# Performance work log

Hardware: AMD Instinct MI355X
Metric: run time of the kernel (lower is better)

Reference implementation:

```python
import jax, jax.numpy as jnp
import numpy as np

B, LQ, LK, D = 8, 2048, 2048, 1024


def setup_inputs() -> dict:
    key = jax.random.key(0)
    k1, k2, k3, k4, k5 = jax.random.split(key, 5)
    inp = jax.random.normal(k1, (B, LQ, D), dtype=jnp.float32)
    memory = jax.random.normal(k2, (B, LK, D), dtype=jnp.float32)
    # 0/1 float mask over memory positions (1 = masked out)
    mask = (jax.random.uniform(k3, (B, LK)) < 0.15).astype(jnp.float32)
    # nn.Linear(D, 1, bias=False): weight shape [1, D], kaiming-uniform-ish init
    w_input = jax.random.uniform(k4, (1, D), dtype=jnp.float32,
                                 minval=-1.0 / np.sqrt(D), maxval=1.0 / np.sqrt(D))
    # dot_scale ~ U(0, 1/sqrt(D)) per original .uniform_(1/input_size**0.5)
    dot_scale = jax.random.uniform(k5, (D,), dtype=jnp.float32,
                                   minval=0.0, maxval=1.0 / np.sqrt(D))
    return {"input": inp, "memory": memory, "mask": mask,
            "w_input": w_input, "dot_scale": dot_scale}


def reference(input, memory, mask, w_input, dot_scale):
    # input_dot: Linear(D,1,bias=False) -> [B, Lq, 1]
    input_dot = jnp.einsum('bqd,od->bqo', input, w_input)  # o == 1
    # cross_dot: (input * dot_scale) @ memory^T -> [B, Lq, Lk]
    cross_dot = jnp.einsum('bqd,bkd->bqk', input * dot_scale, memory)
    att = input_dot + cross_dot - 1e30 * mask[:, None, :]
    weight_one = jax.nn.softmax(att, axis=-1)  # [B, Lq, Lk]
    output_one = jnp.einsum('bqk,bkd->bqd', weight_one, memory)
    return output_one
```

## Files before the change

kernel.cpp:

```cpp
#include <hip/hip_runtime.h>

#define B_  8
#define LQ_ 2048
#define LK_ 2048
#define D_  1024

typedef unsigned short u16;
using short8  = __attribute__((ext_vector_type(8))) short;
using floatx4 = __attribute__((ext_vector_type(4))) float;

#define GAS __attribute__((address_space(1)))
#define LAS __attribute__((address_space(3)))

__device__ __forceinline__ u16 f2bf(float f) {
  unsigned u = __float_as_uint(f);
  u += 0x7fffu + ((u >> 16) & 1u);
  return (u16)(u >> 16);
}
__device__ __forceinline__ float bf2f(u16 h) {
  return __uint_as_float(((unsigned)h) << 16);
}

__global__ void prep(const float* __restrict__ in, const float* __restrict__ mem,
                     const float* __restrict__ ds, u16* __restrict__ qb,
                     u16* __restrict__ mb, u16* __restrict__ mbT) {
  __shared__ u16 tile[64][68];
  int tid = threadIdx.x;
  int tx = tid & 15, ty = tid >> 4;
  int b = blockIdx.z;

  if (blockIdx.y < 16) {
    int k0 = blockIdx.x * 64, d0 = blockIdx.y * 64;
    const float* mB = mem + (size_t)b * LK_ * D_;
    u16* mbB = mb  + (size_t)b * LK_ * D_;
    u16* mtB = mbT + (size_t)b * D_ * LK_;
#pragma unroll
    for (int i = 0; i < 4; i++) {
      int r = ty + 16 * i;
      float4 v = *(const float4*)(mB + (size_t)(k0 + r) * D_ + d0 + tx * 4);
      ushort4 h;
      h.x = f2bf(v.x); h.y = f2bf(v.y); h.z = f2bf(v.z); h.w = f2bf(v.w);
      *(ushort4*)(mbB + (size_t)(k0 + r) * D_ + d0 + tx * 4) = h;
      *(ushort4*)(&tile[r][tx * 4]) = h;
    }
    __syncthreads();
#pragma unroll
    for (int i = 0; i < 4; i++) {
      int rr = ty + 16 * i;
      ushort4 o;
      o.x = tile[tx * 4 + 0][rr];
      o.y = tile[tx * 4 + 1][rr];
      o.z = tile[tx * 4 + 2][rr];
      o.w = tile[tx * 4 + 3][rr];
      *(ushort4*)(mtB + (size_t)(d0 + rr) * LK_ + k0 + tx * 4) = o;
    }
  } else {
    int q0 = blockIdx.x * 64, d0 = (blockIdx.y - 16) * 64;
    const float* iB = in + (size_t)b * LQ_ * D_;
    u16* qB = qb + (size_t)b * LQ_ * D_;
    float4 s4 = *(const float4*)(ds + d0 + tx * 4);
#pragma unroll
    for (int i = 0; i < 4; i++) {
      int r = ty + 16 * i;
      float4 v = *(const float4*)(iB + (size_t)(q0 + r) * D_ + d0 + tx * 4);
      ushort4 h;
      h.x = f2bf(v.x * s4.x); h.y = f2bf(v.y * s4.y);
      h.z = f2bf(v.z * s4.z); h.w = f2bf(v.w * s4.w);
      *(ushort4*)(qB + (size_t)(q0 + r) * D_ + d0 + tx * 4) = h;
    }
  }
}

template <int MODE>
__global__ void gemm_bt(const u16* __restrict__ A, const u16* __restrict__ Bm,
                        void* __restrict__ C, const float* __restrict__ mask,
                        int K, int lda, int ldb, int ldc,
                        size_t sA, size_t sB, size_t sC) {
  __shared__ __align__(16) u16 As[128 * 32];
  __shared__ __align__(16) u16 Bs[128 * 32];
  int tid = threadIdx.x;
  int lane = tid & 63, w = tid >> 6;
  int wm = (w >> 1) * 64, wn = (w & 1) * 64;
  int lm = lane & 15, quad = lane >> 4;

  int tiles_n = gridDim.x;
  int bid = (blockIdx.z * gridDim.y + blockIdx.y) * tiles_n + blockIdx.x;
  int bz = bid & 7;
  int s = bid >> 3;
  const int GM = 8;
  int per_group = GM * tiles_n;
  int group = s / per_group;
  int rem = s - group * per_group;
  int tm = group * GM + (rem & (GM - 1));
  int tn = rem >> 3;

  const u16* Ab = A  + (size_t)bz * sA + (size_t)(tm * 128) * lda;
  const u16* Bb = Bm + (size_t)bz * sB + (size_t)(tn * 128) * ldb;

  int c0 = tid, c1 = tid + 256;
  const u16* gA0 = Ab + (size_t)(c0 >> 2) * lda + (c0 & 3) * 8;
  const u16* gA1 = Ab + (size_t)(c1 >> 2) * lda + (c1 & 3) * 8;
  const u16* gB0 = Bb + (size_t)(c0 >> 2) * ldb + (c0 & 3) * 8;
  const u16* gB1 = Bb + (size_t)(c1 >> 2) * ldb + (c1 & 3) * 8;
  u16* lA0 = As + c0 * 8; u16* lA1 = As + c1 * 8;
  u16* lB0 = Bs + c0 * 8; u16* lB1 = Bs + c1 * 8;

  floatx4 acc[4][4];
#pragma unroll
  for (int mi = 0; mi < 4; mi++)
#pragma unroll
    for (int ni = 0; ni < 4; ni++)
      acc[mi][ni] = {0.f, 0.f, 0.f, 0.f};

  float rs[4] = {0.f, 0.f, 0.f, 0.f};

  for (int k0 = 0; k0 < K; k0 += 32) {
    __builtin_amdgcn_global_load_lds((GAS void*)(gA0 + k0), (LAS void*)lA0, 16, 0, 0);
    __builtin_amdgcn_global_load_lds((GAS void*)(gA1 + k0), (LAS void*)lA1, 16, 0, 0);
    __builtin_amdgcn_global_load_lds((GAS void*)(gB0 + k0), (LAS void*)lB0, 16, 0, 0);
    __builtin_amdgcn_global_load_lds((GAS void*)(gB1 + k0), (LAS void*)lB1, 16, 0, 0);
    __syncthreads();

    short8 af[4], bf[4];
#pragma unroll
    for (int mi = 0; mi < 4; mi++)
      af[mi] = *(const short8*)(As + ((wm + mi * 16 + lm) << 5) + (quad << 3));
#pragma unroll
    for (int ni = 0; ni < 4; ni++)
      bf[ni] = *(const short8*)(Bs + ((wn + ni * 16 + lm) << 5) + (quad << 3));

    if constexpr (MODE == 0) {
#pragma unroll
      for (int mi = 0; mi < 4; mi++) {
        uint4 u = *(const uint4*)&af[mi];
        rs[mi] += __uint_as_float(u.x << 16) + __uint_as_float(u.x & 0xffff0000u)
                + __uint_as_float(u.y << 16) + __uint_as_float(u.y & 0xffff0000u)
                + __uint_as_float(u.z << 16) + __uint_as_float(u.z & 0xffff0000u)
                + __uint_as_float(u.w << 16) + __uint_as_float(u.w & 0xffff0000u);
      }
    }

#pragma unroll
    for (int mi = 0; mi < 4; mi++)
#pragma unroll
      for (int ni = 0; ni < 4; ni++)
        acc[mi][ni] = __builtin_amdgcn_mfma_f32_16x16x32_bf16(af[mi], bf[ni],
                                                              acc[mi][ni], 0, 0, 0);
    __syncthreads();
  }

  int gm0 = tm * 128 + wm + quad * 4;
  int gn0 = tn * 128 + wn + lm;
  size_t cb = (size_t)bz * sC;

  bool msk[4];
  float inv[4];
  if constexpr (MODE == 1) {
    const float* mrow = mask + (size_t)bz * LK_;
#pragma unroll
    for (int ni = 0; ni < 4; ni++) msk[ni] = (mrow[gn0 + ni * 16] != 0.0f);
  } else {
#pragma unroll
    for (int mi = 0; mi < 4; mi++) {
      rs[mi] += __shfl_xor(rs[mi], 16, 64);
      rs[mi] += __shfl_xor(rs[mi], 32, 64);
      inv[mi] = 1.0f / rs[mi];
    }
  }

#pragma unroll
  for (int mi = 0; mi < 4; mi++) {
#pragma unroll
    for (int r = 0; r < 4; r++) {
      size_t rowoff = cb + (size_t)(gm0 + mi * 16 + r) * ldc + gn0;
      float is;
      if constexpr (MODE == 0)
        is = __shfl(inv[mi], quad * 4 + r, 64);
#pragma unroll
      for (int ni = 0; ni < 4; ni++) {
        float v = acc[mi][ni][r];
        if constexpr (MODE == 1)
          ((u16*)C)[rowoff + ni * 16] = msk[ni] ? (u16)0 : f2bf(__expf(v));
        else
          ((float*)C)[rowoff + ni * 16] = v * is;
      }
    }
  }
}

extern "C" void kernel_launch(void* const* d_in, const int* in_sizes, int n_in,
                              void* d_out, int out_size, void* d_ws, size_t ws_size,
                              hipStream_t stream) {
  const float* input  = (const float*)d_in[0];
  const float* memory = (const float*)d_in[1];
  const float* mask   = (const float*)d_in[2];
  const float* dscale = (const float*)d_in[4];

  char* ws = (char*)d_ws;
  u16* qb  = (u16*)(ws);
  u16* mb  = (u16*)(ws + (size_t)32 * 1024 * 1024);
  u16* mbT = (u16*)(ws + (size_t)64 * 1024 * 1024);
  u16* E   = (u16*)(ws + (size_t)96 * 1024 * 1024);
  float* out = (float*)d_out;

  hipLaunchKernelGGL(prep, dim3(32, 32, B_), dim3(256), 0, stream,
                     input, memory, dscale, qb, mb, mbT);
  hipLaunchKernelGGL((gemm_bt<1>), dim3(LK_ / 128, LQ_ / 128, B_), dim3(256), 0,
                     stream, qb, mb, (void*)E, mask, D_, D_, D_, LK_,
                     (size_t)LQ_ * D_, (size_t)LK_ * D_, (size_t)LQ_ * LK_);
  hipLaunchKernelGGL((gemm_bt<0>), dim3(D_ / 128, LQ_ / 128, B_), dim3(256), 0,
                     stream, E, mbT, (void*)out, nullptr, LK_, LK_, LK_, D_,
                     (size_t)LQ_ * LK_, (size_t)D_ * LK_, (size_t)LQ_ * D_);
}
```

Baseline: 342.1 us.

## Double GEMM K-step and move softmax row sums into first GEMM epilogue

The GEMM main loop now loads a 64-wide K slice per barrier pair instead of 32, which halves the number of syncthreads and doubles LDS per block. The softmax denominator is now computed in the exp epilogue of the first GEMM. It uses wave shuffles plus atomicAdd into a workspace buffer that prep zeroes, so the second GEMM no longer unpacks and sums A fragments in its inner loop. The old in-loop row-sum path is kept as a fallback when the workspace is too small. The costs are atomics, an extra global read per row in the second epilogue, and possible occupancy loss from the doubled shared memory.

```diff
diff --git a/kernel.cpp b/kernel.cpp
--- a/kernel.cpp
+++ b/kernel.cpp
@@ -23,11 +23,20 @@
 
 __global__ void prep(const float* __restrict__ in, const float* __restrict__ mem,
                      const float* __restrict__ ds, u16* __restrict__ qb,
-                     u16* __restrict__ mb, u16* __restrict__ mbT) {
+                     u16* __restrict__ mb, u16* __restrict__ mbT,
+                     float* __restrict__ denom) {
   __shared__ u16 tile[64][68];
   int tid = threadIdx.x;
   int tx = tid & 15, ty = tid >> 4;
   int b = blockIdx.z;
+
+  if (denom && blockIdx.y == 16 && blockIdx.x == 0 && blockIdx.z == 0) {
+    float4 z = {0.f, 0.f, 0.f, 0.f};
+    float4* d4 = (float4*)denom;
+#pragma unroll
+    for (int i = 0; i < (B_ * LQ_ / 4) / 256; i++)
+      d4[tid + i * 256] = z;
+  }
 
   if (blockIdx.y < 16) {
     int k0 = blockIdx.x * 64, d0 = blockIdx.y * 64;
@@ -74,10 +83,11 @@
 template <int MODE>
 __global__ void gemm_bt(const u16* __restrict__ A, const u16* __restrict__ Bm,
                         void* __restrict__ C, const float* __restrict__ mask,
-                        int K, int lda, int ldb, int ldc,
+                        float* __restrict__ denom,
+                        int K, int ld, int ldc,
                         size_t sA, size_t sB, size_t sC) {
-  __shared__ __align__(16) u16 As[128 * 32];
-  __shared__ __align__(16) u16 Bs[128 * 32];
+  __shared__ __align__(16) u16 As[128 * 64];
+  __shared__ __align__(16) u16 Bs[128 * 64];
   int tid = threadIdx.x;
   int lane = tid & 63, w = tid >> 6;
   int wm = (w >> 1) * 64, wn = (w & 1) * 64;
@@ -94,16 +104,21 @@
   int tm = group * GM + (rem & (GM - 1));
   int tn = rem >> 3;
 
-  const u16* Ab = A  + (size_t)bz * sA + (size_t)(tm * 128) * lda;
-  const u16* Bb = Bm + (size_t)bz * sB + (size_t)(tn * 128) * ldb;
-
-  int c0 = tid, c1 = tid + 256;
-  const u16* gA0 = Ab + (size_t)(c0 >> 2) * lda + (c0 & 3) * 8;
-  const u16* gA1 = Ab + (size_t)(c1 >> 2) * lda + (c1 & 3) * 8;
-  const u16* gB0 = Bb + (size_t)(c0 >> 2) * ldb + (c0 & 3) * 8;
-  const u16* gB1 = Bb + (size_t)(c1 >> 2) * ldb + (c1 & 3) * 8;
-  u16* lA0 = As + c0 * 8; u16* lA1 = As + c1 * 8;
-  u16* lB0 = Bs + c0 * 8; u16* lB1 = Bs + c1 * 8;
+  const u16* Ab = A  + (size_t)bz * sA + (size_t)(tm * 128) * ld;
+  const u16* Bb = Bm + (size_t)bz * sB + (size_t)(tn * 128) * ld;
+
+  size_t goff[4];
+  u16 *lA[4], *lB[4];
+#pragma unroll
+  for (int j = 0; j < 4; j++) {
+    int c = tid + 256 * j;
+    int half = c >> 9;
+    int row = (c & 511) >> 2;
+    int ko = half * 32 + (c & 3) * 8;
+    goff[j] = (size_t)row * ld + ko;
+    lA[j] = As + c * 8;
+    lB[j] = Bs + c * 8;
+  }
 
   floatx4 acc[4][4];
 #pragma unroll
@@ -114,38 +129,46 @@
 
   float rs[4] = {0.f, 0.f, 0.f, 0.f};
 
-  for (int k0 = 0; k0 < K; k0 += 32) {
-    __builtin_amdgcn_global_load_lds((GAS void*)(gA0 + k0), (LAS void*)lA0, 16, 0, 0);
-    __builtin_amdgcn_global_load_lds((GAS void*)(gA1 + k0), (LAS void*)lA1, 16, 0, 0);
-    __builtin_amdgcn_global_load_lds((GAS void*)(gB0 + k0), (LAS void*)lB0, 16, 0, 0);
-    __builtin_amdgcn_global_load_lds((GAS void*)(gB1 + k0), (LAS void*)lB1, 16, 0, 0);
+  for (int k0 = 0; k0 < K; k0 += 64) {
+#pragma unroll
+    for (int j = 0; j < 4; j++) {
+      __builtin_amdgcn_global_load_lds((GAS void*)(Ab + goff[j] + k0),
+                                       (LAS void*)lA[j], 16, 0, 0);
+      __builtin_amdgcn_global_load_lds((GAS void*)(Bb + goff[j] + k0),
+                                       (LAS void*)lB[j], 16, 0, 0);
+    }
     __syncthreads();
 
-    short8 af[4], bf[4];
-#pragma unroll
-    for (int mi = 0; mi < 4; mi++)
-      af[mi] = *(const short8*)(As + ((wm + mi * 16 + lm) << 5) + (quad << 3));
-#pragma unroll
-    for (int ni = 0; ni < 4; ni++)
-      bf[ni] = *(const short8*)(Bs + ((wn + ni * 16 + lm) << 5) + (quad << 3));
-
-    if constexpr (MODE == 0) {
-#pragma unroll
-      for (int mi = 0; mi < 4; mi++) {
-        uint4 u = *(const uint4*)&af[mi];
-        rs[mi] += __uint_as_float(u.x << 16) + __uint_as_float(u.x & 0xffff0000u)
-                + __uint_as_float(u.y << 16) + __uint_as_float(u.y & 0xffff0000u)
-                + __uint_as_float(u.z << 16) + __uint_as_float(u.z & 0xffff0000u)
-                + __uint_as_float(u.w << 16) + __uint_as_float(u.w & 0xffff0000u);
-      }
-    }
-
-#pragma unroll
-    for (int mi = 0; mi < 4; mi++)
+#pragma unroll
+    for (int kk = 0; kk < 2; kk++) {
+      const u16* Ah = As + kk * 4096;
+      const u16* Bh = Bs + kk * 4096;
+      short8 af[4], bf[4];
+#pragma unroll
+      for (int mi = 0; mi < 4; mi++)
+        af[mi] = *(const short8*)(Ah + ((wm + mi * 16 + lm) << 5) + (quad << 3));
 #pragma unroll
       for (int ni = 0; ni < 4; ni++)
-        acc[mi][ni] = __builtin_amdgcn_mfma_f32_16x16x32_bf16(af[mi], bf[ni],
-                                                              acc[mi][ni], 0, 0, 0);
+        bf[ni] = *(const short8*)(Bh + ((wn + ni * 16 + lm) << 5) + (quad << 3));
+
+      if constexpr (MODE == 2) {
+#pragma unroll
+        for (int mi = 0; mi < 4; mi++) {
+          uint4 u = *(const uint4*)&af[mi];
+          rs[mi] += __uint_as_float(u.x << 16) + __uint_as_float(u.x & 0xffff0000u)
+                  + __uint_as_float(u.y << 16) + __uint_as_float(u.y & 0xffff0000u)
+                  + __uint_as_float(u.z << 16) + __uint_as_float(u.z & 0xffff0000u)
+                  + __uint_as_float(u.w << 16) + __uint_as_float(u.w & 0xffff0000u);
+        }
+      }
+
+#pragma unroll
+      for (int mi = 0; mi < 4; mi++)
+#pragma unroll
+        for (int ni = 0; ni < 4; ni++)
+          acc[mi][ni] = __builtin_amdgcn_mfma_f32_16x16x32_bf16(af[mi], bf[ni],
+                                                                acc[mi][ni], 0, 0, 0);
+    }
     __syncthreads();
   }
 
@@ -153,36 +176,64 @@
   int gn0 = tn * 128 + wn + lm;
   size_t cb = (size_t)bz * sC;
 
-  bool msk[4];
-  float inv[4];
   if constexpr (MODE == 1) {
     const float* mrow = mask + (size_t)bz * LK_;
+    bool msk[4];
 #pragma unroll
     for (int ni = 0; ni < 4; ni++) msk[ni] = (mrow[gn0 + ni * 16] != 0.0f);
+#pragma unroll
+    for (int mi = 0; mi < 4; mi++) {
+#pragma unroll
+      for (int r = 0; r < 4; r++) {
+        int row = gm0 + mi * 16 + r;
+        size_t rowoff = cb + (size_t)row * ldc + gn0;
+        float part = 0.f;
+#pragma unroll
+        for (int ni = 0; ni < 4; ni++) {
+          float e = msk[ni] ? 0.f : __expf(acc[mi][ni][r]);
+          u16 h = f2bf(e);
+          ((u16*)C)[rowoff + ni * 16] = h;
+          part += bf2f(h);
+        }
+        if (denom) {
+          part += __shfl_xor(part, 1, 64);
+          part += __shfl_xor(part, 2, 64);
+          part += __shfl_xor(part, 4, 64);
+          part += __shfl_xor(part, 8, 64);
+          if (lm == 0) atomicAdd(&denom[(size_t)bz * LQ_ + row], part);
+        }
+      }
+    }
+  } else if constexpr (MODE == 0) {
+#pragma unroll
+    for (int mi = 0; mi < 4; mi++) {
+#pragma unroll
+      for (int r = 0; r < 4; r++) {
+        int row = gm0 + mi * 16 + r;
+        float is = 1.0f / denom[(size_t)bz * LQ_ + row];
+        size_t rowoff = cb + (size_t)row * ldc + gn0;
+#pragma unroll
+        for (int ni = 0; ni < 4; ni++)
+          ((float*)C)[rowoff + ni * 16] = acc[mi][ni][r] * is;
+      }
+    }
   } else {
+    float inv[4];
 #pragma unroll
     for (int mi = 0; mi < 4; mi++) {
       rs[mi] += __shfl_xor(rs[mi], 16, 64);
       rs[mi] += __shfl_xor(rs[mi], 32, 64);
       inv[mi] = 1.0f / rs[mi];
     }
-  }
-
-#pragma unroll
-  for (int mi = 0; mi < 4; mi++) {
-#pragma unroll
-    for (int r = 0; r < 4; r++) {
-      size_t rowoff = cb + (size_t)(gm0 + mi * 16 + r) * ldc + gn0;
-      float is;
-      if constexpr (MODE == 0)
-        is = __shfl(inv[mi], quad * 4 + r, 64);
-#pragma unroll
-      for (int ni = 0; ni < 4; ni++) {
-        float v = acc[mi][ni][r];
-        if constexpr (MODE == 1)
-          ((u16*)C)[rowoff + ni * 16] = msk[ni] ? (u16)0 : f2bf(__expf(v));
-        else
-          ((float*)C)[rowoff + ni * 16] = v * is;
+#pragma unroll
+    for (int mi = 0; mi < 4; mi++) {
+#pragma unroll
+      for (int r = 0; r < 4; r++) {
+        size_t rowoff = cb + (size_t)(gm0 + mi * 16 + r) * ldc + gn0;
+        float is = __shfl(inv[mi], quad * 4 + r, 64);
+#pragma unroll
+        for (int ni = 0; ni < 4; ni++)
+          ((float*)C)[rowoff + ni * 16] = acc[mi][ni][r] * is;
       }
     }
   }
@@ -201,14 +252,22 @@
   u16* mb  = (u16*)(ws + (size_t)32 * 1024 * 1024);
   u16* mbT = (u16*)(ws + (size_t)64 * 1024 * 1024);
   u16* E   = (u16*)(ws + (size_t)96 * 1024 * 1024);
+  size_t base = (size_t)160 * 1024 * 1024;
+  bool have_denom = ws_size >= base + (size_t)B_ * LQ_ * sizeof(float);
+  float* denom = have_denom ? (float*)(ws + base) : nullptr;
   float* out = (float*)d_out;
 
   hipLaunchKernelGGL(prep, dim3(32, 32, B_), dim3(256), 0, stream,
-                     input, memory, dscale, qb, mb, mbT);
+                     input, memory, dscale, qb, mb, mbT, denom);
   hipLaunchKernelGGL((gemm_bt<1>), dim3(LK_ / 128, LQ_ / 128, B_), dim3(256), 0,
-                     stream, qb, mb, (void*)E, mask, D_, D_, D_, LK_,
+                     stream, qb, mb, (void*)E, mask, denom, D_, D_, LK_,
                      (size_t)LQ_ * D_, (size_t)LK_ * D_, (size_t)LQ_ * LK_);
-  hipLaunchKernelGGL((gemm_bt<0>), dim3(D_ / 128, LQ_ / 128, B_), dim3(256), 0,
-                     stream, E, mbT, (void*)out, nullptr, LK_, LK_, LK_, D_,
-                     (size_t)LQ_ * LK_, (size_t)D_ * LK_, (size_t)LQ_ * D_);
-}
+  if (have_denom)
+    hipLaunchKernelGGL((gemm_bt<0>), dim3(D_ / 128, LQ_ / 128, B_), dim3(256), 0,
+                       stream, E, mbT, (void*)out, nullptr, denom, LK_, LK_, D_,
+                       (size_t)LQ_ * LK_, (size_t)D_ * LK_, (size_t)LQ_ * D_);
+  else
+    hipLaunchKernelGGL((gemm_bt<2>), dim3(D_ / 128, LQ_ / 128, B_), dim3(256), 0,
+                       stream, E, mbT, (void*)out, nullptr, nullptr, LK_, LK_, D_,
+                       (size_t)LQ_ * LK_, (size_t)D_ * LK_, (size_t)LQ_ * D_);
+}
```

Result: faster. 327.2 us (-4.4%).
